# Optimization experiments

Hardware: AMD Instinct MI355X
Metric: run time of the kernel (lower is better)

## Reference

```python
import jax, jax.numpy as jnp
import numpy as np

EPS = 1e-5  # torch.nn.LayerNorm default

def _layer_norm(h):
    # elementwise_affine=False LayerNorm over last dim
    mu = jnp.mean(h, axis=-1, keepdims=True)
    var = jnp.mean(jnp.square(h - mu), axis=-1, keepdims=True)
    return (h - mu) * jax.lax.rsqrt(var + EPS)

def setup_inputs() -> dict:
    key = jax.random.key(0)
    ks = jax.random.split(key, 5)
    N, D = 2048, 1024
    x = jax.random.normal(ks[0], (N, D), dtype=jnp.float32)
    scale = 0.02
    w_q = jax.random.normal(ks[1], (D, D), dtype=jnp.float32) * scale
    w_k = jax.random.normal(ks[2], (D, D), dtype=jnp.float32) * scale
    w_v = jax.random.normal(ks[3], (D, D), dtype=jnp.float32) * scale
    w_o = jax.random.normal(ks[4], (D, D), dtype=jnp.float32) * scale
    return {"x": x, "w_q": w_q, "w_k": w_k, "w_v": w_v, "w_o": w_o}

def reference(x, w_q, w_k, w_v, w_o):
    N, D = x.shape
    H = 16
    dh = D // H
    xn = _layer_norm(x)
    # per-head projections -> [H, N, dh]
    q = _layer_norm((xn @ w_q).reshape(N, H, dh)).astype(jnp.float16).transpose(1, 0, 2)
    k = _layer_norm((xn @ w_k).reshape(N, H, dh)).astype(jnp.float16).transpose(1, 0, 2)
    v = (xn @ w_v).reshape(N, H, dh).transpose(1, 0, 2)
    sm_scale = 1.0 / jnp.sqrt(jnp.float32(dh))  # flex_attention default scale
    scores = jnp.einsum('hqd,hkd->hqk', q, k, preferred_element_type=jnp.float32) * sm_scale
    # block-sparse pattern: q_idx // 16 == kv_idx % 16 (empty rows for q_idx >= 256)
    idx = jnp.arange(N)
    mask = (idx[:, None] // 16) == (idx[None, :] % 16)  # [N, N]
    neg = jnp.float32(-1e30)
    smax = jnp.max(jnp.where(mask, scores, neg), axis=-1, keepdims=True)
    p = jnp.where(mask, jnp.exp(scores - smax), 0.0)  # [H, N, N]
    denom = jnp.sum(p, axis=-1, keepdims=True)
    # flash-style semantics: fully masked rows output 0
    attn = jnp.einsum('hqk,hkd->hqd', p, v) / jnp.maximum(denom, 1e-30)
    outs = attn.transpose(1, 0, 2).reshape(N, D).astype(jnp.float32)
    return x + outs @ w_o
```

## Files before the change

### kernel.cpp

```cpp
#include <hip/hip_runtime.h>
#include <hip/hip_bf16.h>

typedef unsigned short u16;
typedef __attribute__((ext_vector_type(8))) __bf16 bf16x8;
typedef __attribute__((ext_vector_type(4))) float f32x4;
typedef __attribute__((ext_vector_type(4))) unsigned short u16x4;

#define DEV static __device__ __forceinline__

static constexpr int N = 2048, D = 1024;
static constexpr float EPS = 1e-5f;

DEV u16 f2b(float f) {
  union { float f; unsigned u; } x; x.f = f;
  unsigned r = x.u + 0x7FFFu + ((x.u >> 16) & 1u);
  return (u16)(r >> 16);
}
DEV float b2f(u16 h) {
  union { unsigned u; float f; } x; x.u = ((unsigned)h) << 16;
  return x.f;
}

DEV void async16(const void* g, void* l) {
  __builtin_amdgcn_global_load_lds(
      (const __attribute__((address_space(1))) unsigned int*)g,
      (__attribute__((address_space(3))) unsigned int*)l, 16, 0, 0);
}

__global__ __launch_bounds__(256) void k_pre(const float* __restrict__ x,
                                             const float* __restrict__ wq, const float* __restrict__ wk,
                                             const float* __restrict__ wv, const float* __restrict__ wo,
                                             u16* __restrict__ xn, u16* __restrict__ wt) {
  const int t = threadIdx.x;
  if (blockIdx.x < 2048) {
    const int row = blockIdx.x;
    const float4 v = ((const float4*)(x + (size_t)row * D))[t];
    float s  = v.x + v.y + v.z + v.w;
    float ss = v.x * v.x + v.y * v.y + v.z * v.z + v.w * v.w;
    __shared__ float red0[4], red1[4];
    for (int off = 32; off; off >>= 1) { s += __shfl_xor(s, off, 64); ss += __shfl_xor(ss, off, 64); }
    const int w = t >> 6, l = t & 63;
    if (l == 0) { red0[w] = s; red1[w] = ss; }
    __syncthreads();
    s  = red0[0] + red0[1] + red0[2] + red0[3];
    ss = red1[0] + red1[1] + red1[2] + red1[3];
    const float mu = s * (1.0f / D);
    const float var = ss * (1.0f / D) - mu * mu;
    const float rs = rsqrtf(var + EPS);
    u16x4 o;
    o.x = f2b((v.x - mu) * rs); o.y = f2b((v.y - mu) * rs);
    o.z = f2b((v.z - mu) * rs); o.w = f2b((v.w - mu) * rs);
    ((u16x4*)(xn + (size_t)row * D))[t] = o;
  } else {
    const int bid = blockIdx.x - 2048;
    const int z = bid >> 10, rem = bid & 1023;
    const float* src = z == 0 ? wq : z == 1 ? wk : z == 2 ? wv : wo;
    u16* dst = wt + (size_t)z * D * D;
    __shared__ float tile[32][33];
    const int k0 = (rem >> 5) * 32, n0 = (rem & 31) * 32;
    const int c = t & 31, r4 = t >> 5;
#pragma unroll
    for (int p = 0; p < 4; ++p) { int r = r4 + p * 8; tile[r][c] = src[(size_t)(k0 + r) * D + n0 + c]; }
    __syncthreads();
#pragma unroll
    for (int p = 0; p < 4; ++p) { int r = r4 + p * 8; dst[(size_t)(n0 + r) * D + k0 + c] = f2b(tile[c][r]); }
  }
}

template<int BN>
DEV void gemm_tile(const u16* __restrict__ A, const u16* __restrict__ BT,
                   float* __restrict__ C, int row0, int col0, int ldc, int kbeg, int kend) {
  constexpr int K = 1024, BK = 32, NJ = BN / 32;
  __shared__ __align__(16) u16 As[128 * BK];
  __shared__ __align__(16) u16 Bs[BN * BK];
  const int t = threadIdx.x;
  const int w = t >> 6, l = t & 63;
  const int wm = (w & 1) << 6, wn = (w >> 1) * (BN / 2);

  f32x4 acc[4][NJ];
#pragma unroll
  for (int i = 0; i < 4; ++i)
#pragma unroll
    for (int j = 0; j < NJ; ++j) acc[i][j] = (f32x4){0.f, 0.f, 0.f, 0.f};

  const int sr = t >> 2;
  const int sc = (t & 3) << 3;
  const u16* gA0 = A + (size_t)(row0 + sr) * K + sc;
  const u16* gA1 = gA0 + (size_t)64 * K;
  const u16* gB0 = BT + (size_t)(col0 + sr) * K + sc;
  const u16* gB1 = gB0 + (size_t)64 * K;
  u16* lA0 = &As[sr * BK + sc];
  u16* lA1 = &As[(sr + 64) * BK + sc];
  u16* lB0 = &Bs[sr * BK + sc];
  u16* lB1 = &Bs[(sr + 64) * BK + sc];

  const int fr = l & 15;
  const int kc = (l >> 4) << 3;

  for (int k0 = kbeg; k0 < kend; k0 += BK) {
    async16(gA0 + k0, lA0);
    async16(gA1 + k0, lA1);
    async16(gB0 + k0, lB0);
    if constexpr (BN == 128) async16(gB1 + k0, lB1);
    __syncthreads();
    bf16x8 af[4], bfr[NJ];
#pragma unroll
    for (int i = 0; i < 4; ++i) af[i] = *(const bf16x8*)&As[(wm + i * 16 + fr) * BK + kc];
#pragma unroll
    for (int j = 0; j < NJ; ++j) bfr[j] = *(const bf16x8*)&Bs[(wn + j * 16 + fr) * BK + kc];
#pragma unroll
    for (int i = 0; i < 4; ++i)
#pragma unroll
      for (int j = 0; j < NJ; ++j)
        acc[i][j] = __builtin_amdgcn_mfma_f32_16x16x32_bf16(af[i], bfr[j], acc[i][j], 0, 0, 0);
    __syncthreads();
  }

  const int rq = (l >> 4) << 2;
#pragma unroll
  for (int i = 0; i < 4; ++i)
#pragma unroll
    for (int j = 0; j < NJ; ++j) {
      const int col = col0 + wn + j * 16 + fr;
#pragma unroll
      for (int r = 0; r < 4; ++r) {
        const int row = row0 + wm + i * 16 + rq + r;
        C[(size_t)row * ldc + col] = acc[i][j][r];
      }
    }
}

__global__ __launch_bounds__(256) void k_gemm_qkv(const u16* __restrict__ xn, const u16* __restrict__ wt,
                                                  float* __restrict__ kvb, float* __restrict__ qb) {
  const int bid = blockIdx.x;
  const u16* BT; float* C; int r0, c0, ldc;
  if (bid < 512) { BT = wt + (size_t)D * D; C = kvb; r0 = (bid >> 5) * 128; c0 = (bid & 31) * 64; ldc = 2 * D; }
  else { const int q = bid - 512; BT = wt; C = qb; r0 = (q >> 4) * 128; c0 = (q & 15) * 64; ldc = D; }
  gemm_tile<64>(xn, BT, C, r0, c0, ldc, 0, 1024);
}

__global__ __launch_bounds__(256) void k_gemm_o(const u16* __restrict__ attnb, const u16* __restrict__ wt,
                                                float* __restrict__ part) {
  const int bid = blockIdx.x;
  const int tile = bid & 15, s = bid >> 4;
  const int bm = tile >> 3, bn = tile & 7;
  gemm_tile<128>(attnb, wt + (size_t)3 * D * D, part + (size_t)s * 256 * D,
                 bm * 128, bn * 128, D, s * 128, s * 128 + 128);
}

__global__ __launch_bounds__(256) void k_attn(const float* __restrict__ qb, const float* __restrict__ kvb,
                                              u16* __restrict__ attnb) {
  const int h = blockIdx.x >> 4, b = blockIdx.x & 15;
  __shared__ float q_s[16][68];
  __shared__ u16  k_u[128][68];
  __shared__ u16  v_u[128][64];
  __shared__ float s_s[16][132];
  __shared__ float inv_den[16];
  const int t = threadIdx.x;

  {
    const int i = t >> 4, sub = t & 15;
    const float4 qv = *(const float4*)&qb[(size_t)(b * 16 + i) * D + h * 64 + sub * 4];
    float s  = qv.x + qv.y + qv.z + qv.w;
    float ss = qv.x * qv.x + qv.y * qv.y + qv.z * qv.z + qv.w * qv.w;
    for (int off = 1; off < 16; off <<= 1) { s += __shfl_xor(s, off, 16); ss += __shfl_xor(ss, off, 16); }
    const float mu = s * (1.0f / 64);
    const float var = ss * (1.0f / 64) - mu * mu;
    const float rs = rsqrtf(var + EPS);
    q_s[i][sub * 4 + 0] = (qv.x - mu) * rs;
    q_s[i][sub * 4 + 1] = (qv.y - mu) * rs;
    q_s[i][sub * 4 + 2] = (qv.z - mu) * rs;
    q_s[i][sub * 4 + 3] = (qv.w - mu) * rs;
  }
  {
    const int j = t >> 1, half = t & 1;
    const int kr = b + 16 * j;
    const float4* krow = (const float4*)&kvb[(size_t)kr * (2 * D) + h * 64 + half * 32];
    float4 kv4[8];
    float s = 0.f, ss = 0.f;
#pragma unroll
    for (int c = 0; c < 8; ++c) {
      const float4 vv = krow[c]; kv4[c] = vv;
      s += vv.x + vv.y + vv.z + vv.w;
      ss += vv.x * vv.x + vv.y * vv.y + vv.z * vv.z + vv.w * vv.w;
    }
    s += __shfl_xor(s, 1, 64); ss += __shfl_xor(ss, 1, 64);
    const float mu = s * (1.0f / 64);
    const float var = ss * (1.0f / 64) - mu * mu;
    const float rs = rsqrtf(var + EPS);
#pragma unroll
    for (int c = 0; c < 8; ++c) {
      u16x4 o;
      o.x = f2b((kv4[c].x - mu) * rs); o.y = f2b((kv4[c].y - mu) * rs);
      o.z = f2b((kv4[c].z - mu) * rs); o.w = f2b((kv4[c].w - mu) * rs);
      *(u16x4*)&k_u[j][half * 32 + c * 4] = o;
    }
  }
  {
#pragma unroll
    for (int it = 0; it < 8; ++it) {
      const int idx = t + it * 256;
      const int j = idx >> 4, c = idx & 15;
      const int kr = b + 16 * j;
      const float4 vv = *(const float4*)&kvb[(size_t)kr * (2 * D) + D + h * 64 + c * 4];
      u16x4 o; o.x = f2b(vv.x); o.y = f2b(vv.y); o.z = f2b(vv.z); o.w = f2b(vv.w);
      *(u16x4*)&v_u[j][c * 4] = o;
    }
  }
  __syncthreads();

  const int i = t >> 4;
  const int sub = t & 15;
#pragma unroll
  for (int jj = 0; jj < 8; ++jj) {
    const int j = sub + 16 * jj;
    float acc = 0.f;
#pragma unroll
    for (int d = 0; d < 64; ++d) acc += q_s[i][d] * b2f(k_u[j][d]);
    s_s[i][j] = acc * 0.125f;
  }
  __syncthreads();
  float m = -1e30f;
#pragma unroll
  for (int jj = 0; jj < 8; ++jj) m = fmaxf(m, s_s[i][sub + 16 * jj]);
  for (int off = 1; off < 16; off <<= 1) m = fmaxf(m, __shfl_xor(m, off, 64));
  float sum = 0.f;
#pragma unroll
  for (int jj = 0; jj < 8; ++jj) {
    const int j = sub + 16 * jj;
    const float p = __expf(s_s[i][j] - m);
    s_s[i][j] = p;
    sum += p;
  }
  for (int off = 1; off < 16; off <<= 1) sum += __shfl_xor(sum, off, 64);
  if (sub == 0) inv_den[i] = 1.0f / sum;
  __syncthreads();

  const int db = sub << 2;
  float a0 = 0, a1 = 0, a2 = 0, a3 = 0;
  for (int j = 0; j < 128; ++j) {
    const float p = s_s[i][j];
    a0 += p * b2f(v_u[j][db + 0]);
    a1 += p * b2f(v_u[j][db + 1]);
    a2 += p * b2f(v_u[j][db + 2]);
    a3 += p * b2f(v_u[j][db + 3]);
  }
  const float inv = inv_den[i];
  u16x4 o;
  o.x = f2b(a0 * inv); o.y = f2b(a1 * inv); o.z = f2b(a2 * inv); o.w = f2b(a3 * inv);
  *(u16x4*)&attnb[(size_t)(b * 16 + i) * D + h * 64 + db] = o;
}

__global__ __launch_bounds__(256) void k_finish(const float* __restrict__ x, const float* __restrict__ part,
                                                float* __restrict__ out) {
  const int row = blockIdx.x, t = threadIdx.x;
  float4 v = ((const float4*)(x + (size_t)row * D))[t];
  if (row < 256) {
#pragma unroll
    for (int s = 0; s < 8; ++s) {
      const float4 p = ((const float4*)(part + ((size_t)s * 256 + row) * D))[t];
      v.x += p.x; v.y += p.y; v.z += p.z; v.w += p.w;
    }
  }
  ((float4*)(out + (size_t)row * D))[t] = v;
}

extern "C" void kernel_launch(void* const* d_in, const int* in_sizes, int n_in,
                              void* d_out, int out_size, void* d_ws, size_t ws_size,
                              hipStream_t stream) {
  const float* x  = (const float*)d_in[0];
  const float* wq = (const float*)d_in[1];
  const float* wk = (const float*)d_in[2];
  const float* wv = (const float*)d_in[3];
  const float* wo = (const float*)d_in[4];
  float* out = (float*)d_out;
  char* ws = (char*)d_ws;

  u16*   xn    = (u16*)(ws + 0);
  u16*   wt    = (u16*)(ws + 4194304);
  float* kvb   = (float*)(ws + 12582912);
  float* qb    = (float*)(ws + 29360128);
  float* part  = (float*)(ws + 30408704);
  u16*   attnb = (u16*)(ws + 38797312);

  k_pre<<<dim3(6144), dim3(256), 0, stream>>>(x, wq, wk, wv, wo, xn, wt);
  k_gemm_qkv<<<dim3(544), dim3(256), 0, stream>>>(xn, wt, kvb, qb);
  k_attn<<<dim3(256), dim3(256), 0, stream>>>(qb, kvb, attnb);
  k_gemm_o<<<dim3(128), dim3(256), 0, stream>>>(attnb, wt, part);
  k_finish<<<dim3(2048), dim3(256), 0, stream>>>(x, part, out);
}
```

Baseline: 65.50 us.

## Fuse per-head LayerNorm into QKV GEMM epilogue and double-buffer GEMM loads

The GEMM tile is rewritten with double-buffered async LDS loads and an XOR-swizzled shared layout. The Q/K per-head LayerNorm now runs in the GEMM epilogue through a cross-wave reduction in shared memory, and Q/K/V are stored as bf16 instead of fp32. This cuts intermediate traffic and lets the attention kernel copy them with wide vector loads. The residual copy moves into the prenorm kernel and the O projection atomically adds split-K partials into the output, which removes the finish kernel. Float atomics make the output sum order nondeterministic, and correctness depends on k_pre writing out before k_gemm_o accumulates into it.

Measured after the change: 81.79 us. +24.9%, slower.

```diff
diff --git a/kernel.cpp b/kernel.cpp
--- a/kernel.cpp
+++ b/kernel.cpp
@@ -5,6 +5,7 @@
 typedef __attribute__((ext_vector_type(8))) __bf16 bf16x8;
 typedef __attribute__((ext_vector_type(4))) float f32x4;
 typedef __attribute__((ext_vector_type(4))) unsigned short u16x4;
+typedef __attribute__((ext_vector_type(4))) unsigned int u32x4;
 
 #define DEV static __device__ __forceinline__
 
@@ -30,11 +31,13 @@
 __global__ __launch_bounds__(256) void k_pre(const float* __restrict__ x,
                                              const float* __restrict__ wq, const float* __restrict__ wk,
                                              const float* __restrict__ wv, const float* __restrict__ wo,
-                                             u16* __restrict__ xn, u16* __restrict__ wt) {
+                                             u16* __restrict__ xn, u16* __restrict__ wt,
+                                             float* __restrict__ out) {
   const int t = threadIdx.x;
   if (blockIdx.x < 2048) {
     const int row = blockIdx.x;
     const float4 v = ((const float4*)(x + (size_t)row * D))[t];
+    ((float4*)(out + (size_t)row * D))[t] = v;
     float s  = v.x + v.y + v.z + v.w;
     float ss = v.x * v.x + v.y * v.y + v.z * v.z + v.w * v.w;
     __shared__ float red0[4], red1[4];
@@ -67,92 +70,168 @@
   }
 }
 
-template<int BN>
-DEV void gemm_tile(const u16* __restrict__ A, const u16* __restrict__ BT,
-                   float* __restrict__ C, int row0, int col0, int ldc, int kbeg, int kend) {
-  constexpr int K = 1024, BK = 32, NJ = BN / 32;
-  __shared__ __align__(16) u16 As[128 * BK];
-  __shared__ __align__(16) u16 Bs[BN * BK];
+struct GemmShared {
+  u16 As[2][128 * 32];
+  u16 Bs[2][64 * 32];
+  float red_s[128][2];
+  float red_ss[128][2];
+};
+
+template<int EPI>
+DEV void gemm64(GemmShared& sh, const u16* __restrict__ A, const u16* __restrict__ BT,
+                void* __restrict__ dst, int row0, int col0, int dcol0, int ldc, int kbeg, int kend) {
+  constexpr int K = 1024, BK = 32;
   const int t = threadIdx.x;
   const int w = t >> 6, l = t & 63;
-  const int wm = (w & 1) << 6, wn = (w >> 1) * (BN / 2);
-
-  f32x4 acc[4][NJ];
+  const int wm = (w & 1) << 6, wn = (w >> 1) << 5;
+
+  f32x4 acc[4][2];
 #pragma unroll
   for (int i = 0; i < 4; ++i)
 #pragma unroll
-    for (int j = 0; j < NJ; ++j) acc[i][j] = (f32x4){0.f, 0.f, 0.f, 0.f};
+    for (int j = 0; j < 2; ++j) acc[i][j] = (f32x4){0.f, 0.f, 0.f, 0.f};
 
   const int sr = t >> 2;
-  const int sc = (t & 3) << 3;
-  const u16* gA0 = A + (size_t)(row0 + sr) * K + sc;
+  const int scg = ((t & 3) ^ (sr & 3)) << 3;
+  const u16* gA0 = A + (size_t)(row0 + sr) * K + scg;
   const u16* gA1 = gA0 + (size_t)64 * K;
-  const u16* gB0 = BT + (size_t)(col0 + sr) * K + sc;
-  const u16* gB1 = gB0 + (size_t)64 * K;
-  u16* lA0 = &As[sr * BK + sc];
-  u16* lA1 = &As[(sr + 64) * BK + sc];
-  u16* lB0 = &Bs[sr * BK + sc];
-  u16* lB1 = &Bs[(sr + 64) * BK + sc];
+  const u16* gB0 = BT + (size_t)(col0 + sr) * K + scg;
+  u16* lA0 = &sh.As[0][0] + t * 8;
+  u16* lA1 = lA0 + 64 * BK;
+  u16* lB0 = &sh.Bs[0][0] + t * 8;
+  constexpr int ABUF = 128 * BK, BBUF = 64 * BK;
 
   const int fr = l & 15;
-  const int kc = (l >> 4) << 3;
-
+  const int kg = l >> 4;
+
+  async16(gA0 + kbeg, lA0);
+  async16(gA1 + kbeg, lA1);
+  async16(gB0 + kbeg, lB0);
+  __syncthreads();
+
+  int cur = 0;
   for (int k0 = kbeg; k0 < kend; k0 += BK) {
-    async16(gA0 + k0, lA0);
-    async16(gA1 + k0, lA1);
-    async16(gB0 + k0, lB0);
-    if constexpr (BN == 128) async16(gB1 + k0, lB1);
+    const int nxt = k0 + BK;
+    if (nxt < kend) {
+      const int o = (cur ^ 1);
+      async16(gA0 + nxt, lA0 + o * ABUF);
+      async16(gA1 + nxt, lA1 + o * ABUF);
+      async16(gB0 + nxt, lB0 + o * BBUF);
+    }
+    bf16x8 af[4], bf[2];
+#pragma unroll
+    for (int i = 0; i < 4; ++i) {
+      const int R = wm + i * 16 + fr;
+      af[i] = *(const bf16x8*)&sh.As[cur][R * BK + ((kg ^ (R & 3)) << 3)];
+    }
+#pragma unroll
+    for (int j = 0; j < 2; ++j) {
+      const int R = wn + j * 16 + fr;
+      bf[j] = *(const bf16x8*)&sh.Bs[cur][R * BK + ((kg ^ (R & 3)) << 3)];
+    }
+#pragma unroll
+    for (int i = 0; i < 4; ++i)
+#pragma unroll
+      for (int j = 0; j < 2; ++j)
+        acc[i][j] = __builtin_amdgcn_mfma_f32_16x16x32_bf16(af[i], bf[j], acc[i][j], 0, 0, 0);
     __syncthreads();
-    bf16x8 af[4], bfr[NJ];
-#pragma unroll
-    for (int i = 0; i < 4; ++i) af[i] = *(const bf16x8*)&As[(wm + i * 16 + fr) * BK + kc];
-#pragma unroll
-    for (int j = 0; j < NJ; ++j) bfr[j] = *(const bf16x8*)&Bs[(wn + j * 16 + fr) * BK + kc];
-#pragma unroll
-    for (int i = 0; i < 4; ++i)
-#pragma unroll
-      for (int j = 0; j < NJ; ++j)
-        acc[i][j] = __builtin_amdgcn_mfma_f32_16x16x32_bf16(af[i], bfr[j], acc[i][j], 0, 0, 0);
+    cur ^= 1;
+  }
+
+  const int rq = (l >> 4) << 2;
+  if constexpr (EPI == 1) {
+    float ps[4][4], pss[4][4];
+#pragma unroll
+    for (int i = 0; i < 4; ++i)
+#pragma unroll
+      for (int r = 0; r < 4; ++r) {
+        const float a = acc[i][0][r], b = acc[i][1][r];
+        ps[i][r] = a + b; pss[i][r] = a * a + b * b;
+      }
+    for (int off = 1; off < 16; off <<= 1)
+#pragma unroll
+      for (int i = 0; i < 4; ++i)
+#pragma unroll
+        for (int r = 0; r < 4; ++r) {
+          ps[i][r]  += __shfl_xor(ps[i][r],  off, 16);
+          pss[i][r] += __shfl_xor(pss[i][r], off, 16);
+        }
+    if (fr == 0) {
+#pragma unroll
+      for (int i = 0; i < 4; ++i)
+#pragma unroll
+        for (int r = 0; r < 4; ++r) {
+          const int R = wm + i * 16 + rq + r;
+          sh.red_s[R][w >> 1]  = ps[i][r];
+          sh.red_ss[R][w >> 1] = pss[i][r];
+        }
+    }
     __syncthreads();
-  }
-
-  const int rq = (l >> 4) << 2;
-#pragma unroll
-  for (int i = 0; i < 4; ++i)
-#pragma unroll
-    for (int j = 0; j < NJ; ++j) {
-      const int col = col0 + wn + j * 16 + fr;
+    u16* o = (u16*)dst;
+#pragma unroll
+    for (int i = 0; i < 4; ++i)
 #pragma unroll
       for (int r = 0; r < 4; ++r) {
-        const int row = row0 + wm + i * 16 + rq + r;
-        C[(size_t)row * ldc + col] = acc[i][j][r];
+        const int R = wm + i * 16 + rq + r;
+        const float S  = sh.red_s[R][0] + sh.red_s[R][1];
+        const float SS = sh.red_ss[R][0] + sh.red_ss[R][1];
+        const float mu = S * (1.0f / 64);
+        const float rs = rsqrtf(SS * (1.0f / 64) - mu * mu + EPS);
+#pragma unroll
+        for (int j = 0; j < 2; ++j)
+          o[(size_t)(row0 + R) * ldc + dcol0 + wn + j * 16 + fr] = f2b((acc[i][j][r] - mu) * rs);
       }
-    }
+  } else if constexpr (EPI == 2) {
+    u16* o = (u16*)dst;
+#pragma unroll
+    for (int i = 0; i < 4; ++i)
+#pragma unroll
+      for (int j = 0; j < 2; ++j)
+#pragma unroll
+        for (int r = 0; r < 4; ++r)
+          o[(size_t)(row0 + wm + i * 16 + rq + r) * ldc + dcol0 + wn + j * 16 + fr] = f2b(acc[i][j][r]);
+  } else {
+    float* o = (float*)dst;
+#pragma unroll
+    for (int i = 0; i < 4; ++i)
+#pragma unroll
+      for (int j = 0; j < 2; ++j)
+#pragma unroll
+        for (int r = 0; r < 4; ++r)
+          atomicAdd(&o[(size_t)(row0 + wm + i * 16 + rq + r) * ldc + dcol0 + wn + j * 16 + fr],
+                    acc[i][j][r]);
+  }
 }
 
 __global__ __launch_bounds__(256) void k_gemm_qkv(const u16* __restrict__ xn, const u16* __restrict__ wt,
-                                                  float* __restrict__ kvb, float* __restrict__ qb) {
+                                                  u16* __restrict__ qh, u16* __restrict__ kh,
+                                                  u16* __restrict__ vh) {
+  __shared__ GemmShared sh;
   const int bid = blockIdx.x;
-  const u16* BT; float* C; int r0, c0, ldc;
-  if (bid < 512) { BT = wt + (size_t)D * D; C = kvb; r0 = (bid >> 5) * 128; c0 = (bid & 31) * 64; ldc = 2 * D; }
-  else { const int q = bid - 512; BT = wt; C = qb; r0 = (q >> 4) * 128; c0 = (q & 15) * 64; ldc = D; }
-  gemm_tile<64>(xn, BT, C, r0, c0, ldc, 0, 1024);
+  if (bid < 512) {
+    const int r0 = (bid >> 5) * 128, c0 = (bid & 31) * 64;
+    const u16* BT = wt + (size_t)D * D;
+    if (c0 < 1024) gemm64<1>(sh, xn, BT, kh, r0, c0, c0, D, 0, 1024);
+    else           gemm64<2>(sh, xn, BT, vh, r0, c0, c0 - 1024, D, 0, 1024);
+  } else {
+    const int q = bid - 512;
+    gemm64<1>(sh, xn, wt, qh, (q >> 4) * 128, (q & 15) * 64, (q & 15) * 64, D, 0, 1024);
+  }
 }
 
 __global__ __launch_bounds__(256) void k_gemm_o(const u16* __restrict__ attnb, const u16* __restrict__ wt,
-                                                float* __restrict__ part) {
-  const int bid = blockIdx.x;
-  const int tile = bid & 15, s = bid >> 4;
-  const int bm = tile >> 3, bn = tile & 7;
-  gemm_tile<128>(attnb, wt + (size_t)3 * D * D, part + (size_t)s * 256 * D,
-                 bm * 128, bn * 128, D, s * 128, s * 128 + 128);
-}
-
-__global__ __launch_bounds__(256) void k_attn(const float* __restrict__ qb, const float* __restrict__ kvb,
-                                              u16* __restrict__ attnb) {
+                                                float* __restrict__ out) {
+  __shared__ GemmShared sh;
+  const int tile = blockIdx.x & 31, s = blockIdx.x >> 5;
+  gemm64<3>(sh, attnb, wt + (size_t)3 * D * D, out,
+            (tile >> 4) * 128, (tile & 15) * 64, (tile & 15) * 64, D, s * 256, s * 256 + 256);
+}
+
+__global__ __launch_bounds__(256) void k_attn(const u16* __restrict__ qh, const u16* __restrict__ kh,
+                                              const u16* __restrict__ vh, u16* __restrict__ attnb) {
   const int h = blockIdx.x >> 4, b = blockIdx.x & 15;
   __shared__ float q_s[16][68];
-  __shared__ u16  k_u[128][68];
+  __shared__ u16  k_u[128][72];
   __shared__ u16  v_u[128][64];
   __shared__ float s_s[16][132];
   __shared__ float inv_den[16];
@@ -160,52 +239,17 @@
 
   {
     const int i = t >> 4, sub = t & 15;
-    const float4 qv = *(const float4*)&qb[(size_t)(b * 16 + i) * D + h * 64 + sub * 4];
-    float s  = qv.x + qv.y + qv.z + qv.w;
-    float ss = qv.x * qv.x + qv.y * qv.y + qv.z * qv.z + qv.w * qv.w;
-    for (int off = 1; off < 16; off <<= 1) { s += __shfl_xor(s, off, 16); ss += __shfl_xor(ss, off, 16); }
-    const float mu = s * (1.0f / 64);
-    const float var = ss * (1.0f / 64) - mu * mu;
-    const float rs = rsqrtf(var + EPS);
-    q_s[i][sub * 4 + 0] = (qv.x - mu) * rs;
-    q_s[i][sub * 4 + 1] = (qv.y - mu) * rs;
-    q_s[i][sub * 4 + 2] = (qv.z - mu) * rs;
-    q_s[i][sub * 4 + 3] = (qv.w - mu) * rs;
-  }
-  {
-    const int j = t >> 1, half = t & 1;
+    const u16x4 qq = *(const u16x4*)&qh[(size_t)(b * 16 + i) * D + h * 64 + sub * 4];
+    q_s[i][sub * 4 + 0] = b2f(qq.x); q_s[i][sub * 4 + 1] = b2f(qq.y);
+    q_s[i][sub * 4 + 2] = b2f(qq.z); q_s[i][sub * 4 + 3] = b2f(qq.w);
+  }
+#pragma unroll
+  for (int it = 0; it < 4; ++it) {
+    const int idx = t + it * 256;
+    const int j = idx >> 3, c = (idx & 7) * 8;
     const int kr = b + 16 * j;
-    const float4* krow = (const float4*)&kvb[(size_t)kr * (2 * D) + h * 64 + half * 32];
-    float4 kv4[8];
-    float s = 0.f, ss = 0.f;
-#pragma unroll
-    for (int c = 0; c < 8; ++c) {
-      const float4 vv = krow[c]; kv4[c] = vv;
-      s += vv.x + vv.y + vv.z + vv.w;
-      ss += vv.x * vv.x + vv.y * vv.y + vv.z * vv.z + vv.w * vv.w;
-    }
-    s += __shfl_xor(s, 1, 64); ss += __shfl_xor(ss, 1, 64);
-    const float mu = s * (1.0f / 64);
-    const float var = ss * (1.0f / 64) - mu * mu;
-    const float rs = rsqrtf(var + EPS);
-#pragma unroll
-    for (int c = 0; c < 8; ++c) {
-      u16x4 o;
-      o.x = f2b((kv4[c].x - mu) * rs); o.y = f2b((kv4[c].y - mu) * rs);
-      o.z = f2b((kv4[c].z - mu) * rs); o.w = f2b((kv4[c].w - mu) * rs);
-      *(u16x4*)&k_u[j][half * 32 + c * 4] = o;
-    }
-  }
-  {
-#pragma unroll
-    for (int it = 0; it < 8; ++it) {
-      const int idx = t + it * 256;
-      const int j = idx >> 4, c = idx & 15;
-      const int kr = b + 16 * j;
-      const float4 vv = *(const float4*)&kvb[(size_t)kr * (2 * D) + D + h * 64 + c * 4];
-      u16x4 o; o.x = f2b(vv.x); o.y = f2b(vv.y); o.z = f2b(vv.z); o.w = f2b(vv.w);
-      *(u16x4*)&v_u[j][c * 4] = o;
-    }
+    *(u32x4*)&k_u[j][c] = *(const u32x4*)&kh[(size_t)kr * D + h * 64 + c];
+    *(u32x4*)&v_u[j][c] = *(const u32x4*)&vh[(size_t)kr * D + h * 64 + c];
   }
   __syncthreads();
 
@@ -216,7 +260,11 @@
     const int j = sub + 16 * jj;
     float acc = 0.f;
 #pragma unroll
-    for (int d = 0; d < 64; ++d) acc += q_s[i][d] * b2f(k_u[j][d]);
+    for (int d4 = 0; d4 < 16; ++d4) {
+      const u16x4 kk = *(const u16x4*)&k_u[j][d4 * 4];
+      acc += q_s[i][d4 * 4 + 0] * b2f(kk.x) + q_s[i][d4 * 4 + 1] * b2f(kk.y)
+           + q_s[i][d4 * 4 + 2] * b2f(kk.z) + q_s[i][d4 * 4 + 3] * b2f(kk.w);
+    }
     s_s[i][j] = acc * 0.125f;
   }
   __syncthreads();
@@ -240,29 +288,13 @@
   float a0 = 0, a1 = 0, a2 = 0, a3 = 0;
   for (int j = 0; j < 128; ++j) {
     const float p = s_s[i][j];
-    a0 += p * b2f(v_u[j][db + 0]);
-    a1 += p * b2f(v_u[j][db + 1]);
-    a2 += p * b2f(v_u[j][db + 2]);
-    a3 += p * b2f(v_u[j][db + 3]);
+    const u16x4 vv = *(const u16x4*)&v_u[j][db];
+    a0 += p * b2f(vv.x); a1 += p * b2f(vv.y); a2 += p * b2f(vv.z); a3 += p * b2f(vv.w);
   }
   const float inv = inv_den[i];
   u16x4 o;
   o.x = f2b(a0 * inv); o.y = f2b(a1 * inv); o.z = f2b(a2 * inv); o.w = f2b(a3 * inv);
   *(u16x4*)&attnb[(size_t)(b * 16 + i) * D + h * 64 + db] = o;
-}
-
-__global__ __launch_bounds__(256) void k_finish(const float* __restrict__ x, const float* __restrict__ part,
-                                                float* __restrict__ out) {
-  const int row = blockIdx.x, t = threadIdx.x;
-  float4 v = ((const float4*)(x + (size_t)row * D))[t];
-  if (row < 256) {
-#pragma unroll
-    for (int s = 0; s < 8; ++s) {
-      const float4 p = ((const float4*)(part + ((size_t)s * 256 + row) * D))[t];
-      v.x += p.x; v.y += p.y; v.z += p.z; v.w += p.w;
-    }
-  }
-  ((float4*)(out + (size_t)row * D))[t] = v;
 }
 
 extern "C" void kernel_launch(void* const* d_in, const int* in_sizes, int n_in,
@@ -276,16 +308,15 @@
   float* out = (float*)d_out;
   char* ws = (char*)d_ws;
 
-  u16*   xn    = (u16*)(ws + 0);
-  u16*   wt    = (u16*)(ws + 4194304);
-  float* kvb   = (float*)(ws + 12582912);
-  float* qb    = (float*)(ws + 29360128);
-  float* part  = (float*)(ws + 30408704);
-  u16*   attnb = (u16*)(ws + 38797312);
-
-  k_pre<<<dim3(6144), dim3(256), 0, stream>>>(x, wq, wk, wv, wo, xn, wt);
-  k_gemm_qkv<<<dim3(544), dim3(256), 0, stream>>>(xn, wt, kvb, qb);
-  k_attn<<<dim3(256), dim3(256), 0, stream>>>(qb, kvb, attnb);
-  k_gemm_o<<<dim3(128), dim3(256), 0, stream>>>(attnb, wt, part);
-  k_finish<<<dim3(2048), dim3(256), 0, stream>>>(x, part, out);
-}
+  u16* xn    = (u16*)(ws + 0);
+  u16* wt    = (u16*)(ws + 4194304);
+  u16* qh    = (u16*)(ws + 12582912);
+  u16* kh    = (u16*)(ws + 13107200);
+  u16* vh    = (u16*)(ws + 17301504);
+  u16* attnb = (u16*)(ws + 21495808);
+
+  k_pre<<<dim3(6144), dim3(256), 0, stream>>>(x, wq, wk, wv, wo, xn, wt, out);
+  k_gemm_qkv<<<dim3(544), dim3(256), 0, stream>>>(xn, wt, qh, kh, vh);
+  k_attn<<<dim3(256), dim3(256), 0, stream>>>(qh, kh, vh, attnb);
+  k_gemm_o<<<dim3(128), dim3(256), 0, stream>>>(attnb, wt, out);
+}
```
